# Kernel tuning notes

Measured on AMD Instinct MI355X. Metric: run time of the kernel, lower is better.

The kernel has to match this reference:

```python
import jax, jax.numpy as jnp
import numpy as np

# NF4 codebook (QLoRA): 16 quantile values of a standard normal, normalized to [-1, 1]
NF4_TABLE = jnp.array([
    -1.0, -0.6961928009986877, -0.5250730514526367, -0.39491748809814453,
    -0.28444138169288635, -0.18477343022823334, -0.09105003625154495, 0.0,
    0.07958029955625534, 0.16093020141124725, 0.24611230194568634,
    0.33791524171829224, 0.44070982933044434, 0.5626170039176941,
    0.7229568362236328, 1.0], dtype=jnp.float32)

IN_DIM = 4096
OUT_DIM = 4096
RANK = 16
ALPHA = 32.0
BLOCK = 64  # NF4 quantization block size along the flattened weight


def setup_inputs() -> dict:
    key = jax.random.key(0)
    k1, k2, k3, k4, k5 = jax.random.split(key, 5)
    x = jax.random.normal(k1, (4, 2048, IN_DIM), dtype=jnp.float32)
    # 4-bit codes into NF4_TABLE, stored unpacked as int32
    w_codes = jax.random.randint(k2, (OUT_DIM, IN_DIM), 0, 16, dtype=jnp.int32)
    # per-block absmax scales (positive)
    w_scales = jax.random.uniform(k3, (OUT_DIM, IN_DIM // BLOCK), dtype=jnp.float32) * 0.02 + 1e-3
    # lora_a: kaiming-uniform-ish scale; lora_b: nonzero for testability (original inits to zeros)
    lora_a = jax.random.normal(k4, (RANK, IN_DIM), dtype=jnp.float32) * (1.0 / np.sqrt(IN_DIM))
    lora_b = jax.random.normal(k5, (OUT_DIM, RANK), dtype=jnp.float32) * 0.01
    return {"x": x, "w_codes": w_codes, "w_scales": w_scales, "lora_a": lora_a, "lora_b": lora_b}


def _dequant_nf4(w_codes, w_scales):
    # codes [O, I] -> dequantized weight [O, I]
    w = NF4_TABLE[w_codes]                                   # [O, I]
    w = w.reshape(OUT_DIM, IN_DIM // BLOCK, BLOCK) * w_scales[:, :, None]
    return w.reshape(OUT_DIM, IN_DIM)


def reference(x, w_codes, w_scales, lora_a, lora_b):
    # base: frozen NF4 linear (dequantize then matmul), no bias
    w = _dequant_nf4(w_codes, w_scales)                      # [O, I]
    base = jnp.einsum('bsi,oi->bso', x, w)                   # [B, S, O]
    # LoRA path: dropout p=0.0 -> identity; scale alpha / rank
    ax = jnp.einsum('bsi,ri->bsr', x, lora_a)                # [B, S, r]
    lora = jnp.einsum('bsr,or->bso', ax, lora_b)             # [B, S, O]
    return base + (ALPHA / RANK) * lora
```

## Files before the change

kernel.cpp:

```cpp
#include <hip/hip_runtime.h>
#include <hip/hip_bf16.h>


#define IN_DIM  4096
#define OUT_DIM 4096
#define RANK    16
#define M_TOK   8192
#define LORA_SCALE 2.0f

typedef __bf16 bf16_t;
typedef bf16_t bf16x8 __attribute__((ext_vector_type(8)));
typedef float  f32x4  __attribute__((ext_vector_type(4)));

__device__ __constant__ float NF4_TAB[16] = {
    -1.0f, -0.6961928009986877f, -0.5250730514526367f, -0.39491748809814453f,
    -0.28444138169288635f, -0.18477343022823334f, -0.09105003625154495f, 0.0f,
    0.07958029955625534f, 0.16093020141124725f, 0.24611230194568634f,
    0.33791524171829224f, 0.44070982933044434f, 0.5626170039176941f,
    0.7229568362236328f, 1.0f};

__global__ __launch_bounds__(256) void prep_w(
    const int* __restrict__ codes,
    const float* __restrict__ scales,
    const float* __restrict__ la,
    const float* __restrict__ lb,
    bf16_t* __restrict__ W)
{
    __shared__ float nf4s[16];
    __shared__ float lbs[4][16];
    const int o0 = blockIdx.x * 4;
    const int tid = threadIdx.x;
    if (tid < 64) lbs[tid >> 4][tid & 15] = lb[(o0 + (tid >> 4)) * RANK + (tid & 15)] * LORA_SCALE;
    else if (tid < 80) nf4s[tid - 64] = NF4_TAB[tid - 64];
    __syncthreads();

    #pragma unroll
    for (int it = 0; it < 2; ++it) {
        const int i0 = (it * 256 + tid) * 8;
        float w[4][8];
        #pragma unroll
        for (int oo = 0; oo < 4; ++oo) {
            const size_t base = (size_t)(o0 + oo) * IN_DIM + i0;
            int4 c0 = *(const int4*)(codes + base);
            int4 c1 = *(const int4*)(codes + base + 4);
            const float sc = scales[(o0 + oo) * (IN_DIM / 64) + (i0 >> 6)];
            w[oo][0] = nf4s[c0.x] * sc; w[oo][1] = nf4s[c0.y] * sc;
            w[oo][2] = nf4s[c0.z] * sc; w[oo][3] = nf4s[c0.w] * sc;
            w[oo][4] = nf4s[c1.x] * sc; w[oo][5] = nf4s[c1.y] * sc;
            w[oo][6] = nf4s[c1.z] * sc; w[oo][7] = nf4s[c1.w] * sc;
        }
        #pragma unroll
        for (int r = 0; r < RANK; ++r) {
            float4 a0 = *(const float4*)(la + r * IN_DIM + i0);
            float4 a1 = *(const float4*)(la + r * IN_DIM + i0 + 4);
            #pragma unroll
            for (int oo = 0; oo < 4; ++oo) {
                const float b = lbs[oo][r];
                w[oo][0] += b * a0.x; w[oo][1] += b * a0.y;
                w[oo][2] += b * a0.z; w[oo][3] += b * a0.w;
                w[oo][4] += b * a1.x; w[oo][5] += b * a1.y;
                w[oo][6] += b * a1.z; w[oo][7] += b * a1.w;
            }
        }
        #pragma unroll
        for (int oo = 0; oo < 4; ++oo) {
            bf16x8 v;
            #pragma unroll
            for (int j = 0; j < 8; ++j) v[j] = (bf16_t)w[oo][j];
            *(bf16x8*)(W + (size_t)(o0 + oo) * IN_DIM + i0) = v;
        }
    }
}

__global__ __launch_bounds__(256) void cast_x(
    const float* __restrict__ x, bf16_t* __restrict__ y, int n8)
{
    const int stride = gridDim.x * blockDim.x;
    for (int i = blockIdx.x * blockDim.x + threadIdx.x; i < n8; i += stride) {
        const size_t e = (size_t)i * 8;
        float4 a = *(const float4*)(x + e);
        float4 b = *(const float4*)(x + e + 4);
        bf16x8 v;
        v[0] = (bf16_t)a.x; v[1] = (bf16_t)a.y; v[2] = (bf16_t)a.z; v[3] = (bf16_t)a.w;
        v[4] = (bf16_t)b.x; v[5] = (bf16_t)b.y; v[6] = (bf16_t)b.z; v[7] = (bf16_t)b.w;
        *(bf16x8*)(y + e) = v;
    }
}

#define BM 256
#define BN 256
#define BK 32
#define NT (IN_DIM / BK)

__global__ __launch_bounds__(512, 2) void gemm_bt(
    const bf16_t* __restrict__ A, const bf16_t* __restrict__ B,
    float* __restrict__ C)
{
    __shared__ bf16_t lds[4][2][BM * BK];

    const int tid  = threadIdx.x;
    const int wave = tid >> 6;
    const int lane = tid & 63;

    const int flat = blockIdx.y * gridDim.x + blockIdx.x;
    const int swz  = (flat & 7) * 64 + (flat >> 3);
    const int bx = swz & 15;
    const int by = swz >> 4;
    const int m0 = by * BM;
    const int n0 = bx * BN;

    const int wr = wave >> 2;
    const int wc = wave & 3;

    f32x4 acc[8][4];
    #pragma unroll
    for (int i = 0; i < 8; ++i)
        #pragma unroll
        for (int j = 0; j < 4; ++j) acc[i][j] = (f32x4)0.0f;

    const size_t KB = (size_t)IN_DIM * 2;

    int s_row[2], s_gc[2];
    #pragma unroll
    for (int p = 0; p < 2; ++p) {
        const int off = p * 8192 + tid * 16;
        s_row[p] = off >> 6;
        s_gc[p]  = ((off >> 4) & 3) ^ ((s_row[p] >> 1) & 3);
    }
    const char* gA = (const char*)A;
    const char* gB = (const char*)B;

    const int frow = lane & 15;
    const int fch  = lane >> 4;
    int offA[8], offB[4];
    #pragma unroll
    for (int i = 0; i < 8; ++i) {
        const int ra = wr * 128 + i * 16 + frow;
        offA[i] = ra * 64 + ((fch ^ ((ra >> 1) & 3)) << 4);
    }
    #pragma unroll
    for (int j = 0; j < 4; ++j) {
        const int rb = wc * 64 + j * 16 + frow;
        offB[j] = rb * 64 + ((fch ^ ((rb >> 1) & 3)) << 4);
    }

#define LD(bidx) ((const char*)&lds[bidx][0][0])

#define STAGE(tt, bidx) do {                                                   \
    const size_t kb_ = (size_t)(tt) * (BK * 2);                                \
    _Pragma("unroll")                                                          \
    for (int p = 0; p < 2; ++p) {                                              \
        const char* srcA = gA + (size_t)(m0 + s_row[p]) * KB + kb_ + (s_gc[p] << 4); \
        const char* srcB = gB + (size_t)(n0 + s_row[p]) * KB + kb_ + (s_gc[p] << 4); \
        char* dA = (char*)&lds[bidx][0][0] + p * 8192 + wave * 1024;           \
        char* dB = (char*)&lds[bidx][1][0] + p * 8192 + wave * 1024;           \
        __builtin_amdgcn_global_load_lds(                                      \
            (const __attribute__((address_space(1))) void*)srcA,               \
            (__attribute__((address_space(3))) void*)dA, 16, 0, 0);            \
        __builtin_amdgcn_global_load_lds(                                      \
            (const __attribute__((address_space(1))) void*)srcB,               \
            (__attribute__((address_space(3))) void*)dB, 16, 0, 0);            \
    }                                                                          \
} while (0)

#define READ_FRAGS(AF, BF, base_) do {                                         \
    const char* bA_ = (base_);                                                 \
    const char* bB_ = (base_) + 16384;                                         \
    _Pragma("unroll")                                                          \
    for (int i = 0; i < 8; ++i) AF[i] = *(const bf16x8*)(bA_ + offA[i]);       \
    _Pragma("unroll")                                                          \
    for (int j = 0; j < 4; ++j) BF[j] = *(const bf16x8*)(bB_ + offB[j]);       \
} while (0)

#define WAIT_LGKM do {                                                         \
    asm volatile("s_waitcnt lgkmcnt(0)" ::: "memory");                         \
    __builtin_amdgcn_sched_barrier(0);                                         \
} while (0)

#define MFMA_HALF(AF, BF, I0) do {                                             \
    __builtin_amdgcn_s_setprio(1);                                             \
    _Pragma("unroll")                                                          \
    for (int i = 0; i < 4; ++i)                                                \
        _Pragma("unroll")                                                      \
        for (int j = 0; j < 4; ++j)                                            \
            acc[(I0) + i][j] = __builtin_amdgcn_mfma_f32_16x16x32_bf16(        \
                AF[(I0) + i], BF[j], acc[(I0) + i][j], 0, 0, 0);               \
    __builtin_amdgcn_s_setprio(0);                                             \
} while (0)

    bf16x8 afE[8], bfE[4], afO[8], bfO[4];

    STAGE(0, 0);
    STAGE(1, 1);
    STAGE(2, 2);
    asm volatile("s_waitcnt vmcnt(8)" ::: "memory");
    __builtin_amdgcn_s_barrier();
    READ_FRAGS(afE, bfE, LD(0));

    for (int t = 0; t < NT - 4; t += 2) {
        STAGE(t + 3, (t + 3) & 3);
        WAIT_LGKM;
        MFMA_HALF(afE, bfE, 0);
        asm volatile("s_waitcnt vmcnt(8)" ::: "memory");
        __builtin_amdgcn_s_barrier();
        READ_FRAGS(afO, bfO, LD((t + 1) & 3));
        MFMA_HALF(afE, bfE, 4);
        STAGE(t + 4, (t + 4) & 3);
        WAIT_LGKM;
        MFMA_HALF(afO, bfO, 0);
        asm volatile("s_waitcnt vmcnt(8)" ::: "memory");
        __builtin_amdgcn_s_barrier();
        READ_FRAGS(afE, bfE, LD((t + 2) & 3));
        MFMA_HALF(afO, bfO, 4);
    }

    STAGE(127, 3);
    WAIT_LGKM;
    MFMA_HALF(afE, bfE, 0);
    asm volatile("s_waitcnt vmcnt(8)" ::: "memory");
    __builtin_amdgcn_s_barrier();
    READ_FRAGS(afO, bfO, LD(1));
    MFMA_HALF(afE, bfE, 4);

    WAIT_LGKM;
    MFMA_HALF(afO, bfO, 0);
    asm volatile("s_waitcnt vmcnt(4)" ::: "memory");
    __builtin_amdgcn_s_barrier();
    READ_FRAGS(afE, bfE, LD(2));
    MFMA_HALF(afO, bfO, 4);

    WAIT_LGKM;
    MFMA_HALF(afE, bfE, 0);
    asm volatile("s_waitcnt vmcnt(0)" ::: "memory");
    __builtin_amdgcn_s_barrier();
    READ_FRAGS(afO, bfO, LD(3));
    MFMA_HALF(afE, bfE, 4);

    WAIT_LGKM;
    MFMA_HALF(afO, bfO, 0);
    MFMA_HALF(afO, bfO, 4);

    const int crow = (lane >> 4) * 4;
    const int ccol = lane & 15;
    #pragma unroll
    for (int i = 0; i < 8; ++i) {
        #pragma unroll
        for (int j = 0; j < 4; ++j) {
            const int mb = m0 + wr * 128 + i * 16 + crow;
            const int nb = n0 + wc * 64 + j * 16 + ccol;
            #pragma unroll
            for (int r = 0; r < 4; ++r)
                C[(size_t)(mb + r) * OUT_DIM + nb] = acc[i][j][r];
        }
    }
#undef STAGE
#undef READ_FRAGS
#undef WAIT_LGKM
#undef MFMA_HALF
#undef LD
}

extern "C" void kernel_launch(void* const* d_in, const int* in_sizes, int n_in,
                              void* d_out, int out_size, void* d_ws, size_t ws_size,
                              hipStream_t stream) {
    const float* x      = (const float*)d_in[0];
    const int*   codes  = (const int*)d_in[1];
    const float* scales = (const float*)d_in[2];
    const float* la     = (const float*)d_in[3];
    const float* lb     = (const float*)d_in[4];
    float* out = (float*)d_out;

    bf16_t* W  = (bf16_t*)d_ws;
    bf16_t* xb = (bf16_t*)((char*)d_ws + (size_t)OUT_DIM * IN_DIM * 2);

    prep_w<<<OUT_DIM / 4, 256, 0, stream>>>(codes, scales, la, lb, W);
    cast_x<<<2048, 256, 0, stream>>>(x, xb, (M_TOK * IN_DIM) / 8);

    dim3 grid(OUT_DIM / BN, M_TOK / BM);
    gemm_bt<<<grid, 512, 0, stream>>>(xb, W, out);
}
```

Before: 288.1 us.

## Restructure GEMM main loop into 8-phase ping-pong schedule with BK=64 LDS slots

Rewrites the bf16 GEMM main loop so each block uses two 64 KB LDS slots holding BK=64 (two 32-wide K halves) for both operands. Each K-half is split into two N-halves, so stage issue, fragment reads and MFMA clusters interleave in eight barrier-separated phases, like the HipKittens-style 8-wave ping-pong. The aim is finer-grained overlap of global-to-LDS loads, LDS reads and MFMA work, with fewer live B-fragment registers. In exchange it uses 128 KB of LDS per block and adds many more barriers per K step, which may cut occupancy to one block per CU and add synchronization cost.

```diff
diff --git a/kernel.cpp b/kernel.cpp
--- a/kernel.cpp
+++ b/kernel.cpp
@@ -20,10 +20,8 @@
     0.7229568362236328f, 1.0f};
 
 __global__ __launch_bounds__(256) void prep_w(
-    const int* __restrict__ codes,
-    const float* __restrict__ scales,
-    const float* __restrict__ la,
-    const float* __restrict__ lb,
+    const int* __restrict__ codes, const float* __restrict__ scales,
+    const float* __restrict__ la, const float* __restrict__ lb,
     bf16_t* __restrict__ W)
 {
     __shared__ float nf4s[16];
@@ -87,16 +85,11 @@
     }
 }
 
-#define BM 256
-#define BN 256
-#define BK 32
-#define NT (IN_DIM / BK)
-
 __global__ __launch_bounds__(512, 2) void gemm_bt(
     const bf16_t* __restrict__ A, const bf16_t* __restrict__ B,
     float* __restrict__ C)
 {
-    __shared__ bf16_t lds[4][2][BM * BK];
+    __shared__ __align__(128) char lds[131072];
 
     const int tid  = threadIdx.x;
     const int wave = tid >> 6;
@@ -106,8 +99,8 @@
     const int swz  = (flat & 7) * 64 + (flat >> 3);
     const int bx = swz & 15;
     const int by = swz >> 4;
-    const int m0 = by * BM;
-    const int n0 = bx * BN;
+    const int m0 = by * 256;
+    const int n0 = bx * 256;
 
     const int wr = wave >> 2;
     const int wc = wave & 3;
@@ -118,127 +111,120 @@
         #pragma unroll
         for (int j = 0; j < 4; ++j) acc[i][j] = (f32x4)0.0f;
 
-    const size_t KB = (size_t)IN_DIM * 2;
-
-    int s_row[2], s_gc[2];
-    #pragma unroll
-    for (int p = 0; p < 2; ++p) {
-        const int off = p * 8192 + tid * 16;
-        s_row[p] = off >> 6;
-        s_gc[p]  = ((off >> 4) & 3) ^ ((s_row[p] >> 1) & 3);
-    }
+    const int frow = lane & 15;
+    const int fch  = lane >> 4;
+
+    int offA[8], offB0[2], offB1[2];
+    #pragma unroll
+    for (int f = 0; f < 8; ++f) {
+        const int r = wr * 128 + f * 16 + frow;
+        offA[f] = r * 64 + ((fch ^ ((r >> 1) & 3)) << 4);
+    }
+    #pragma unroll
+    for (int n = 0; n < 2; ++n) {
+        const int c0 = wc * 64 + n * 16 + frow;
+        offB0[n] = c0 * 64 + ((fch ^ ((c0 >> 1) & 3)) << 4);
+        const int c1 = wc * 64 + 32 + n * 16 + frow;
+        offB1[n] = c1 * 64 + ((fch ^ ((c1 >> 1) & 3)) << 4);
+    }
+
+    const int d0 = tid * 16, d1 = 8192 + tid * 16;
+    const int sr0 = d0 >> 6, sr1 = d1 >> 6;
+    const int sg0 = ((d0 >> 4) & 3) ^ ((sr0 >> 1) & 3);
+    const int sg1 = ((d1 >> 4) & 3) ^ ((sr1 >> 1) & 3);
     const char* gA = (const char*)A;
     const char* gB = (const char*)B;
 
-    const int frow = lane & 15;
-    const int fch  = lane >> 4;
-    int offA[8], offB[4];
-    #pragma unroll
-    for (int i = 0; i < 8; ++i) {
-        const int ra = wr * 128 + i * 16 + frow;
-        offA[i] = ra * 64 + ((fch ^ ((ra >> 1) & 3)) << 4);
-    }
-    #pragma unroll
-    for (int j = 0; j < 4; ++j) {
-        const int rb = wc * 64 + j * 16 + frow;
-        offB[j] = rb * 64 + ((fch ^ ((rb >> 1) & 3)) << 4);
-    }
-
-#define LD(bidx) ((const char*)&lds[bidx][0][0])
-
-#define STAGE(tt, bidx) do {                                                   \
-    const size_t kb_ = (size_t)(tt) * (BK * 2);                                \
+    bf16x8 fA[8], fB0[2], fB1[2];
+
+#define DS_A(SL, KH) do {                                                      \
+    const char* bA_ = lds + (SL) * 65536 + (KH) * 16384;                       \
     _Pragma("unroll")                                                          \
-    for (int p = 0; p < 2; ++p) {                                              \
-        const char* srcA = gA + (size_t)(m0 + s_row[p]) * KB + kb_ + (s_gc[p] << 4); \
-        const char* srcB = gB + (size_t)(n0 + s_row[p]) * KB + kb_ + (s_gc[p] << 4); \
-        char* dA = (char*)&lds[bidx][0][0] + p * 8192 + wave * 1024;           \
-        char* dB = (char*)&lds[bidx][1][0] + p * 8192 + wave * 1024;           \
-        __builtin_amdgcn_global_load_lds(                                      \
-            (const __attribute__((address_space(1))) void*)srcA,               \
-            (__attribute__((address_space(3))) void*)dA, 16, 0, 0);            \
-        __builtin_amdgcn_global_load_lds(                                      \
-            (const __attribute__((address_space(1))) void*)srcB,               \
-            (__attribute__((address_space(3))) void*)dB, 16, 0, 0);            \
-    }                                                                          \
-} while (0)
-
-#define READ_FRAGS(AF, BF, base_) do {                                         \
-    const char* bA_ = (base_);                                                 \
-    const char* bB_ = (base_) + 16384;                                         \
-    _Pragma("unroll")                                                          \
-    for (int i = 0; i < 8; ++i) AF[i] = *(const bf16x8*)(bA_ + offA[i]);       \
-    _Pragma("unroll")                                                          \
-    for (int j = 0; j < 4; ++j) BF[j] = *(const bf16x8*)(bB_ + offB[j]);       \
-} while (0)
-
-#define WAIT_LGKM do {                                                         \
-    asm volatile("s_waitcnt lgkmcnt(0)" ::: "memory");                         \
-    __builtin_amdgcn_sched_barrier(0);                                         \
-} while (0)
-
-#define MFMA_HALF(AF, BF, I0) do {                                             \
+    for (int f_ = 0; f_ < 8; ++f_) fA[f_] = *(const bf16x8*)(bA_ + offA[f_]);  \
+} while (0)
+
+#define DS_B(SL, KH, FB, OFB) do {                                             \
+    const char* bB_ = lds + (SL) * 65536 + 32768 + (KH) * 16384;               \
+    FB[0] = *(const bf16x8*)(bB_ + OFB[0]);                                    \
+    FB[1] = *(const bf16x8*)(bB_ + OFB[1]);                                    \
+} while (0)
+
+#define STG(OPI, KH_, SL, T) do {                                              \
+    const char* g_  = (OPI) ? gB : gA;                                         \
+    const int   r0_ = (OPI) ? n0 : m0;                                         \
+    const size_t ko_ = (size_t)(T) * 128 + (KH_) * 64;                         \
+    const char* s0_ = g_ + (size_t)(r0_ + sr0) * 8192 + ko_ + (sg0 << 4);      \
+    const char* s1_ = g_ + (size_t)(r0_ + sr1) * 8192 + ko_ + (sg1 << 4);      \
+    char* db_ = lds + (SL) * 65536 + (OPI) * 32768 + (KH_) * 16384 + wave * 1024; \
+    __builtin_amdgcn_global_load_lds(                                          \
+        (const __attribute__((address_space(1))) void*)s0_,                    \
+        (__attribute__((address_space(3))) void*)db_, 16, 0, 0);               \
+    __builtin_amdgcn_global_load_lds(                                          \
+        (const __attribute__((address_space(1))) void*)s1_,                    \
+        (__attribute__((address_space(3))) void*)(db_ + 8192), 16, 0, 0);      \
+} while (0)
+
+#define MM(NH, FB) do {                                                        \
     __builtin_amdgcn_s_setprio(1);                                             \
     _Pragma("unroll")                                                          \
-    for (int i = 0; i < 4; ++i)                                                \
-        _Pragma("unroll")                                                      \
-        for (int j = 0; j < 4; ++j)                                            \
-            acc[(I0) + i][j] = __builtin_amdgcn_mfma_f32_16x16x32_bf16(        \
-                AF[(I0) + i], BF[j], acc[(I0) + i][j], 0, 0, 0);               \
+    for (int f_ = 0; f_ < 8; ++f_) {                                           \
+        acc[f_][(NH)*2+0] = __builtin_amdgcn_mfma_f32_16x16x32_bf16(           \
+            fA[f_], FB[0], acc[f_][(NH)*2+0], 0, 0, 0);                        \
+        acc[f_][(NH)*2+1] = __builtin_amdgcn_mfma_f32_16x16x32_bf16(           \
+            fA[f_], FB[1], acc[f_][(NH)*2+1], 0, 0, 0);                        \
+    }                                                                          \
     __builtin_amdgcn_s_setprio(0);                                             \
 } while (0)
 
-    bf16x8 afE[8], bfE[4], afO[8], bfO[4];
-
-    STAGE(0, 0);
-    STAGE(1, 1);
-    STAGE(2, 2);
-    asm volatile("s_waitcnt vmcnt(8)" ::: "memory");
-    __builtin_amdgcn_s_barrier();
-    READ_FRAGS(afE, bfE, LD(0));
-
-    for (int t = 0; t < NT - 4; t += 2) {
-        STAGE(t + 3, (t + 3) & 3);
-        WAIT_LGKM;
-        MFMA_HALF(afE, bfE, 0);
-        asm volatile("s_waitcnt vmcnt(8)" ::: "memory");
-        __builtin_amdgcn_s_barrier();
-        READ_FRAGS(afO, bfO, LD((t + 1) & 3));
-        MFMA_HALF(afE, bfE, 4);
-        STAGE(t + 4, (t + 4) & 3);
-        WAIT_LGKM;
-        MFMA_HALF(afO, bfO, 0);
-        asm volatile("s_waitcnt vmcnt(8)" ::: "memory");
-        __builtin_amdgcn_s_barrier();
-        READ_FRAGS(afE, bfE, LD((t + 2) & 3));
-        MFMA_HALF(afO, bfO, 4);
-    }
-
-    STAGE(127, 3);
-    WAIT_LGKM;
-    MFMA_HALF(afE, bfE, 0);
-    asm volatile("s_waitcnt vmcnt(8)" ::: "memory");
-    __builtin_amdgcn_s_barrier();
-    READ_FRAGS(afO, bfO, LD(1));
-    MFMA_HALF(afE, bfE, 4);
-
-    WAIT_LGKM;
-    MFMA_HALF(afO, bfO, 0);
-    asm volatile("s_waitcnt vmcnt(4)" ::: "memory");
-    __builtin_amdgcn_s_barrier();
-    READ_FRAGS(afE, bfE, LD(2));
-    MFMA_HALF(afO, bfO, 4);
-
-    WAIT_LGKM;
-    MFMA_HALF(afE, bfE, 0);
-    asm volatile("s_waitcnt vmcnt(0)" ::: "memory");
-    __builtin_amdgcn_s_barrier();
-    READ_FRAGS(afO, bfO, LD(3));
-    MFMA_HALF(afE, bfE, 4);
-
-    WAIT_LGKM;
-    MFMA_HALF(afO, bfO, 0);
-    MFMA_HALF(afO, bfO, 4);
+#define BAR __builtin_amdgcn_s_barrier()
+#define LG0 do { asm volatile("s_waitcnt lgkmcnt(0)" ::: "memory");            \
+                 __builtin_amdgcn_sched_barrier(0); } while (0)
+#define VM4 asm volatile("s_waitcnt vmcnt(4)" ::: "memory")
+#define VM0 asm volatile("s_waitcnt vmcnt(0)" ::: "memory")
+
+    STG(0, 0, 0, 0); STG(1, 0, 0, 0); STG(0, 1, 0, 0); STG(1, 1, 0, 0);
+    STG(0, 0, 1, 1); STG(1, 0, 1, 1);
+    VM4;
+    BAR;
+
+    for (int i = 0; i < 31; ++i) {
+        const int tY  = 2 * i + 1;
+        const int tX2 = 2 * i + 2;
+        const int tY2 = 2 * i + 3;
+        DS_A(0, 0); DS_B(0, 0, fB0, offB0); STG(0, 1, 1, tY);
+        BAR; LG0; MM(0, fB0); BAR;
+        DS_B(0, 0, fB1, offB1); STG(1, 1, 1, tY);
+        BAR; LG0; MM(1, fB1); BAR;
+        DS_A(0, 1); DS_B(0, 1, fB0, offB0); STG(0, 0, 0, tX2);
+        BAR; LG0; MM(0, fB0); BAR;
+        DS_B(0, 1, fB1, offB1); STG(1, 0, 0, tX2);
+        VM4; BAR; LG0; MM(1, fB1); BAR;
+        DS_A(1, 0); DS_B(1, 0, fB0, offB0); STG(0, 1, 0, tX2);
+        BAR; LG0; MM(0, fB0); BAR;
+        DS_B(1, 0, fB1, offB1); STG(1, 1, 0, tX2);
+        BAR; LG0; MM(1, fB1); BAR;
+        DS_A(1, 1); DS_B(1, 1, fB0, offB0); STG(0, 0, 1, tY2);
+        BAR; LG0; MM(0, fB0); BAR;
+        DS_B(1, 1, fB1, offB1); STG(1, 0, 1, tY2);
+        VM4; BAR; LG0; MM(1, fB1); BAR;
+    }
+
+    DS_A(0, 0); DS_B(0, 0, fB0, offB0); STG(0, 1, 1, 63);
+    BAR; LG0; MM(0, fB0); BAR;
+    DS_B(0, 0, fB1, offB1); STG(1, 1, 1, 63);
+    BAR; LG0; MM(1, fB1); BAR;
+    DS_A(0, 1); DS_B(0, 1, fB0, offB0);
+    BAR; LG0; MM(0, fB0); BAR;
+    DS_B(0, 1, fB1, offB1);
+    VM0; BAR; LG0; MM(1, fB1); BAR;
+    DS_A(1, 0); DS_B(1, 0, fB0, offB0);
+    BAR; LG0; MM(0, fB0); BAR;
+    DS_B(1, 0, fB1, offB1);
+    BAR; LG0; MM(1, fB1); BAR;
+    DS_A(1, 1); DS_B(1, 1, fB0, offB0);
+    BAR; LG0; MM(0, fB0); BAR;
+    DS_B(1, 1, fB1, offB1);
+    LG0; MM(1, fB1);
 
     const int crow = (lane >> 4) * 4;
     const int ccol = lane & 15;
@@ -253,11 +239,14 @@
                 C[(size_t)(mb + r) * OUT_DIM + nb] = acc[i][j][r];
         }
     }
-#undef STAGE
-#undef READ_FRAGS
-#undef WAIT_LGKM
-#undef MFMA_HALF
-#undef LD
+#undef DS_A
+#undef DS_B
+#undef STG
+#undef MM
+#undef BAR
+#undef LG0
+#undef VM4
+#undef VM0
 }
 
 extern "C" void kernel_launch(void* const* d_in, const int* in_sizes, int n_in,
@@ -276,6 +265,6 @@
     prep_w<<<OUT_DIM / 4, 256, 0, stream>>>(codes, scales, la, lb, W);
     cast_x<<<2048, 256, 0, stream>>>(x, xb, (M_TOK * IN_DIM) / 8);
 
-    dim3 grid(OUT_DIM / BN, M_TOK / BM);
+    dim3 grid(OUT_DIM / 256, M_TOK / 256);
     gemm_bt<<<grid, 512, 0, stream>>>(xb, W, out);
 }
```

Result: slower. 298.3 us (+3.6%).
